# Kernel tuning notes

Hardware: AMD Instinct MI355X
Metric: run time of the kernel (lower is better)

Reference implementation:

```python
import jax, jax.numpy as jnp
import numpy as np

B, L, D = 4, 8192, 256          # batch, seq length, embedding dim
H, HD = 8, 32                   # heads, head dim (H*HD == D)
WN, P, S = 9, 4, 1              # window size, padding, stride
EPS = 1e-5


def _layer_norm(x, g, b):
    m = jnp.mean(x, axis=-1, keepdims=True)
    v = jnp.mean(jnp.square(x - m), axis=-1, keepdims=True)
    return (x - m) / jnp.sqrt(v + EPS) * g + b


def setup_inputs() -> dict:
    key = jax.random.key(0)
    ks = jax.random.split(key, 8)
    sc = 0.05
    return {
        "x": jax.random.normal(ks[0], (B, L, D), jnp.float32),
        "W_q": jax.random.normal(ks[1], (D, D), jnp.float32) * sc,
        "W_k": jax.random.normal(ks[2], (D, D), jnp.float32) * sc,
        "W_v": jax.random.normal(ks[3], (D, D), jnp.float32) * sc,
        "W_o": jax.random.normal(ks[4], (D, D), jnp.float32) * sc,
        "pos": jax.random.normal(ks[5], (WN, D), jnp.float32) * sc,
        "W_out": jax.random.normal(ks[6], (D, D), jnp.float32) * sc,
        "b_out": jnp.zeros((D,), jnp.float32),
        "g1": jnp.ones((D,), jnp.float32),
        "b1": jnp.zeros((D,), jnp.float32),
        "g2": jnp.ones((D,), jnp.float32),
        "b2": jnp.zeros((D,), jnp.float32),
    }


def reference(x, W_q, W_k, W_v, W_o, pos, W_out, b_out, g1, b1, g2, b2):
    # input_dim == embedding_dim -> no input projection
    padded = jnp.pad(x, ((0, 0), (P, P), (0, 0)))
    nw = (L + 2 * P - WN) // S + 1  # == L for S=1, WN=2P+1
    idx = jnp.arange(nw)[:, None] * S + jnp.arange(WN)[None, :]  # [nw, WN]
    win = padded[:, idx] + pos  # [B, nw, WN, D]

    def proj(w):  # [B, nw, WN, H, HD]
        return jnp.einsum('bnwd,de->bnwe', win, w).reshape(B, nw, WN, H, HD)

    q, k, v = proj(W_q), proj(W_k), proj(W_v)
    scale = 1.0 / (HD ** 0.5)
    scores = jnp.einsum('bnqhd,bnkhd->bnhqk', q, k) * scale  # [B,nw,H,WN,WN]
    attn = jax.nn.softmax(scores, axis=-1)
    # context, summed over query positions within each window (use_mean=False)
    ctx = jnp.einsum('bnhqk,bnkhd->bnhd', attn, v).reshape(B, nw, D)
    skip = x[:, ::S]  # [B, nw, D]
    attn_res = _layer_norm(skip + ctx @ W_o, g1, b1)
    out = _layer_norm(attn_res @ W_out.T + b_out + attn_res, g2, b2)
    return jax.nn.relu(out)
```

## Files before the change

kernel.cpp:

```cpp
#include <hip/hip_runtime.h>
#include <hip/hip_bf16.h>
#include <math.h>

constexpr int NB   = 4;
constexpr int LL   = 8192;
constexpr int DD   = 256;
constexpr int NH   = 8;
constexpr int HDIM = 32;
constexpr int WNN  = 9;
constexpr int PPAD = 4;

constexpr int CW  = 32;
constexpr int RSN = CW + 8;
constexpr int SST = 260;

typedef __attribute__((ext_vector_type(8))) short bf16x8;
typedef __attribute__((ext_vector_type(4))) float f32x4;

__device__ inline short f2bf(float f) {
  __hip_bfloat16 h = __float2bfloat16(f);
  short s; __builtin_memcpy(&s, &h, 2); return s;
}
__device__ inline float bf2f(short s) {
  unsigned u = ((unsigned)(unsigned short)s) << 16;
  float f; __builtin_memcpy(&f, &u, 4); return f;
}

__global__ __launch_bounds__(256) void prep_all(
    const float* __restrict__ x, short* __restrict__ XB,
    const float* __restrict__ Wq, const float* __restrict__ Wk, const float* __restrict__ Wv,
    const float* __restrict__ Wo, const float* __restrict__ Wout,
    short* __restrict__ WqT, short* __restrict__ WkT, short* __restrict__ WvT,
    short* __restrict__ WoT, short* __restrict__ WoutB,
    const float* __restrict__ pos,
    short* __restrict__ PQb, short* __restrict__ PKb, short* __restrict__ PVb) {
  __shared__ float ps[256];
  const int t = threadIdx.x;
  const int bx = blockIdx.x;
  if (bx < 4) {
    const float* W = (bx == 0) ? Wq : (bx == 1) ? Wk : (bx == 2) ? Wv : Wo;
    short* T = (bx == 0) ? WqT : (bx == 1) ? WkT : (bx == 2) ? WvT : WoT;
    for (int k = 0; k < 256; k += 4) {
      short4 o;
      o.x = f2bf(W[(size_t)(k + 0) * 256 + t]);
      o.y = f2bf(W[(size_t)(k + 1) * 256 + t]);
      o.z = f2bf(W[(size_t)(k + 2) * 256 + t]);
      o.w = f2bf(W[(size_t)(k + 3) * 256 + t]);
      *(short4*)&T[(size_t)t * 256 + k] = o;
    }
  } else if (bx == 4) {
    for (int i = t; i < 16384; i += 256) {
      float4 v = *(const float4*)(Wout + (size_t)i * 4);
      short4 o; o.x = f2bf(v.x); o.y = f2bf(v.y); o.z = f2bf(v.z); o.w = f2bf(v.w);
      *(short4*)(WoutB + (size_t)i * 4) = o;
    }
  } else if (bx < 32) {
    const int idx = bx - 5;
    const int wrow = idx % WNN, wh = idx / WNN;
    const float* W = (wh == 0) ? Wq : (wh == 1) ? Wk : Wv;
    short* P = (wh == 0) ? PQb : (wh == 1) ? PKb : PVb;
    ps[t] = pos[wrow * 256 + t];
    __syncthreads();
    float a = 0.f;
    for (int d = 0; d < 256; ++d) a += ps[d] * W[(size_t)d * 256 + t];
    P[wrow * 256 + t] = f2bf(a);
  } else {
    size_t i = ((size_t)(bx - 32) * 256 + t) * 4;
    float4 v = *(const float4*)(x + i);
    short4 o; o.x = f2bf(v.x); o.y = f2bf(v.y); o.z = f2bf(v.z); o.w = f2bf(v.w);
    *(short4*)(XB + i) = o;
  }
}

__global__ __launch_bounds__(256) void qkv_mfma(
    const short* __restrict__ XB,
    const short* __restrict__ WT0, const short* __restrict__ WT1, const short* __restrict__ WT2,
    short* __restrict__ O0, short* __restrict__ O1, short* __restrict__ O2) {
  const int t = threadIdx.x, w = t >> 6, lane = t & 63, q = lane >> 4, m = lane & 15;
  const size_t row0 = (size_t)blockIdx.x * 64;
  const short* WT = (blockIdx.y == 0) ? WT0 : (blockIdx.y == 1) ? WT1 : WT2;
  short* O = (blockIdx.y == 0) ? O0 : (blockIdx.y == 1) ? O1 : O2;

  f32x4 acc[4][4];
#pragma unroll
  for (int i = 0; i < 4; ++i)
#pragma unroll
    for (int j = 0; j < 4; ++j) acc[i][j] = (f32x4){0.f, 0.f, 0.f, 0.f};

  const short* abase = XB + (row0 + m) * (size_t)256 + q * 8;
  const short* bbase = WT + (size_t)(w * 64 + m) * 256 + q * 8;
  bf16x8 a[4], b[4];
#pragma unroll
  for (int i = 0; i < 4; ++i) a[i] = *(const bf16x8*)(abase + (size_t)i * 4096);
#pragma unroll
  for (int j = 0; j < 4; ++j) b[j] = *(const bf16x8*)(bbase + (size_t)j * 4096);
#pragma unroll
  for (int kk = 0; kk < 8; ++kk) {
    bf16x8 an[4], bn[4];
    if (kk < 7) {
#pragma unroll
      for (int i = 0; i < 4; ++i) an[i] = *(const bf16x8*)(abase + (size_t)i * 4096 + (kk + 1) * 32);
#pragma unroll
      for (int j = 0; j < 4; ++j) bn[j] = *(const bf16x8*)(bbase + (size_t)j * 4096 + (kk + 1) * 32);
    }
#pragma unroll
    for (int i = 0; i < 4; ++i)
#pragma unroll
      for (int j = 0; j < 4; ++j)
        acc[i][j] = __builtin_amdgcn_mfma_f32_16x16x32_bf16(a[i], b[j], acc[i][j], 0, 0, 0);
    if (kk < 7) {
#pragma unroll
      for (int i = 0; i < 4; ++i) a[i] = an[i];
#pragma unroll
      for (int j = 0; j < 4; ++j) b[j] = bn[j];
    }
  }
#pragma unroll
  for (int i = 0; i < 4; ++i)
#pragma unroll
    for (int j = 0; j < 4; ++j)
#pragma unroll
      for (int r = 0; r < 4; ++r) {
        size_t row = row0 + i * 16 + q * 4 + r;
        int col = w * 64 + j * 16 + m;
        O[row * 256 + col] = f2bf(acc[i][j][r]);
      }
}

__global__ __launch_bounds__(256, 2) void attn_kernel(
    const short* __restrict__ XQb, const short* __restrict__ XKb, const short* __restrict__ XVb,
    const short* __restrict__ PQb, const short* __restrict__ PKb, const short* __restrict__ PVb,
    short* __restrict__ CTXB) {
  __shared__ short sq[RSN * SST];
  __shared__ short sk[RSN * SST];
  __shared__ short sv[RSN * SST];
  __shared__ short pq[WNN * SST];
  __shared__ short pk[WNN * SST];
  __shared__ short pv[WNN * SST];

  const int t = threadIdx.x;
  const int nblk = LL / CW;
  const int b = blockIdx.x / nblk;
  const int n0 = (blockIdx.x % nblk) * CW;
  const size_t base = (size_t)b * LL * DD;

  const int lq   = t & 63;
  const int gcol = ((((lq & 7) << 3) | (lq >> 3))) * 4;
  const int pcol = ((lq >> 3) << 5) | ((lq & 7) << 2);

#pragma unroll
  for (int i = 0; i < RSN / 4; ++i) {
    int r = (t >> 6) + i * 4;
    int j = n0 - PPAD + r;
    short4 vq = {0, 0, 0, 0}, vk = vq, vv = vq;
    if (j >= 0 && j < LL) {
      size_t off = base + (size_t)j * DD + gcol;
      vq = *(const short4*)(XQb + off);
      vk = *(const short4*)(XKb + off);
      vv = *(const short4*)(XVb + off);
    }
    *(short4*)&sq[r * SST + pcol] = vq;
    *(short4*)&sk[r * SST + pcol] = vk;
    *(short4*)&sv[r * SST + pcol] = vv;
  }
#pragma unroll
  for (int i = 0; i < 3; ++i) {
    int r = (t >> 6) + i * 4;
    if (r < WNN) {
      *(short4*)&pq[r * SST + pcol] = *(const short4*)(PQb + r * DD + gcol);
      *(short4*)&pk[r * SST + pcol] = *(const short4*)(PKb + r * DD + gcol);
      *(short4*)&pv[r * SST + pcol] = *(const short4*)(PVb + r * DD + gcol);
    }
  }
  __syncthreads();

  const int n = t >> 3;
  const int h = t & 7;
  const int hoff = h * HDIM;
  const int hph = h * 4;

  float sc[WNN][WNN];
#pragma unroll
  for (int qi = 0; qi < WNN; ++qi)
#pragma unroll
    for (int ki = 0; ki < WNN; ++ki) sc[qi][ki] = 0.f;

#pragma unroll
  for (int c = 0; c < 8; ++c) {
    const int cph = c * 32 + hph;
    float qv[WNN][4], kv[WNN][4];
#pragma unroll
    for (int r = 0; r < WNN; ++r) {
      short4 xa = *(const short4*)&sq[(n + r) * SST + cph];
      short4 pa = *(const short4*)&pq[r * SST + cph];
      qv[r][0] = bf2f(xa.x) + bf2f(pa.x);
      qv[r][1] = bf2f(xa.y) + bf2f(pa.y);
      qv[r][2] = bf2f(xa.z) + bf2f(pa.z);
      qv[r][3] = bf2f(xa.w) + bf2f(pa.w);
      short4 xb = *(const short4*)&sk[(n + r) * SST + cph];
      short4 pb = *(const short4*)&pk[r * SST + cph];
      kv[r][0] = bf2f(xb.x) + bf2f(pb.x);
      kv[r][1] = bf2f(xb.y) + bf2f(pb.y);
      kv[r][2] = bf2f(xb.z) + bf2f(pb.z);
      kv[r][3] = bf2f(xb.w) + bf2f(pb.w);
    }
#pragma unroll
    for (int qi = 0; qi < WNN; ++qi)
#pragma unroll
      for (int ki = 0; ki < WNN; ++ki)
        sc[qi][ki] += qv[qi][0] * kv[ki][0] + qv[qi][1] * kv[ki][1] +
                      qv[qi][2] * kv[ki][2] + qv[qi][3] * kv[ki][3];
  }

  float cs[WNN];
#pragma unroll
  for (int ki = 0; ki < WNN; ++ki) cs[ki] = 0.f;
  const float scale = 0.17677669529663687f;
#pragma unroll
  for (int qi = 0; qi < WNN; ++qi) {
    float mx = sc[qi][0];
#pragma unroll
    for (int ki = 1; ki < WNN; ++ki) mx = fmaxf(mx, sc[qi][ki]);
    float e[WNN], sum = 0.f;
#pragma unroll
    for (int ki = 0; ki < WNN; ++ki) { e[ki] = __expf((sc[qi][ki] - mx) * scale); sum += e[ki]; }
    float inv = 1.f / sum;
#pragma unroll
    for (int ki = 0; ki < WNN; ++ki) cs[ki] += e[ki] * inv;
  }

#pragma unroll
  for (int c = 0; c < 8; ++c) {
    const int cph = c * 32 + hph;
    float o0 = 0.f, o1 = 0.f, o2 = 0.f, o3 = 0.f;
#pragma unroll
    for (int ki = 0; ki < WNN; ++ki) {
      short4 xv4 = *(const short4*)&sv[(n + ki) * SST + cph];
      short4 pv4 = *(const short4*)&pv[ki * SST + cph];
      float wt = cs[ki];
      o0 += wt * (bf2f(xv4.x) + bf2f(pv4.x));
      o1 += wt * (bf2f(xv4.y) + bf2f(pv4.y));
      o2 += wt * (bf2f(xv4.z) + bf2f(pv4.z));
      o3 += wt * (bf2f(xv4.w) + bf2f(pv4.w));
    }
    short4 os; os.x = f2bf(o0); os.y = f2bf(o1); os.z = f2bf(o2); os.w = f2bf(o3);
    *(short4*)(CTXB + base + (size_t)(n0 + n) * DD + hoff + c * 4) = os;
  }
}


__global__ __launch_bounds__(256) void out_mfma(
    const short* __restrict__ CTXB, const float* __restrict__ X,
    const short* __restrict__ WoT, const short* __restrict__ WoutB,
    const float* __restrict__ bo,
    const float* __restrict__ g1, const float* __restrict__ b1,
    const float* __restrict__ g2, const float* __restrict__ b2,
    float* __restrict__ out) {
  __shared__ short ar[64 * 264];
  __shared__ float ws1[64][4], ws2[64][4];
  __shared__ float msh[64], rsh[64];
  __shared__ float g1s[256], b1s[256], g2s[256], b2s[256], bos[256];
  const int t = threadIdx.x, w = t >> 6, lane = t & 63, q = lane >> 4, m = lane & 15;
  const size_t row0 = (size_t)blockIdx.x * 64;
  g1s[t] = g1[t]; b1s[t] = b1[t]; g2s[t] = g2[t]; b2s[t] = b2[t]; bos[t] = bo[t];

  f32x4 acc[4][4];
#pragma unroll
  for (int i = 0; i < 4; ++i)
#pragma unroll
    for (int j = 0; j < 4; ++j) acc[i][j] = (f32x4){0.f, 0.f, 0.f, 0.f};

  const short* abase = CTXB + (row0 + m) * (size_t)256 + q * 8;
  const short* bbase = WoT + (size_t)(w * 64 + m) * 256 + q * 8;
  {
    bf16x8 a[4], b[4];
#pragma unroll
    for (int i = 0; i < 4; ++i) a[i] = *(const bf16x8*)(abase + (size_t)i * 4096);
#pragma unroll
    for (int j = 0; j < 4; ++j) b[j] = *(const bf16x8*)(bbase + (size_t)j * 4096);
#pragma unroll
    for (int kk = 0; kk < 8; ++kk) {
      bf16x8 an[4], bn[4];
      if (kk < 7) {
#pragma unroll
        for (int i = 0; i < 4; ++i) an[i] = *(const bf16x8*)(abase + (size_t)i * 4096 + (kk + 1) * 32);
#pragma unroll
        for (int j = 0; j < 4; ++j) bn[j] = *(const bf16x8*)(bbase + (size_t)j * 4096 + (kk + 1) * 32);
      }
#pragma unroll
      for (int i = 0; i < 4; ++i)
#pragma unroll
        for (int j = 0; j < 4; ++j)
          acc[i][j] = __builtin_amdgcn_mfma_f32_16x16x32_bf16(a[i], b[j], acc[i][j], 0, 0, 0);
      if (kk < 7) {
#pragma unroll
        for (int i = 0; i < 4; ++i) a[i] = an[i];
#pragma unroll
        for (int j = 0; j < 4; ++j) b[j] = bn[j];
      }
    }
  }

  float s1v[4][4], s2v[4][4];
#pragma unroll
  for (int i = 0; i < 4; ++i)
#pragma unroll
    for (int r = 0; r < 4; ++r) {
      float a0 = 0.f, b0 = 0.f;
#pragma unroll
      for (int j = 0; j < 4; ++j) {
        float v = acc[i][j][r] + X[(row0 + i * 16 + q * 4 + r) * 256 + w * 64 + j * 16 + m];
        acc[i][j][r] = v; a0 += v; b0 += v * v;
      }
      s1v[i][r] = a0; s2v[i][r] = b0;
    }
#pragma unroll
  for (int i = 0; i < 4; ++i)
#pragma unroll
    for (int r = 0; r < 4; ++r)
#pragma unroll
      for (int msk = 1; msk < 16; msk <<= 1) {
        s1v[i][r] += __shfl_xor(s1v[i][r], msk, 64);
        s2v[i][r] += __shfl_xor(s2v[i][r], msk, 64);
      }
  if (m == 0) {
#pragma unroll
    for (int i = 0; i < 4; ++i)
#pragma unroll
      for (int r = 0; r < 4; ++r) {
        ws1[i * 16 + q * 4 + r][w] = s1v[i][r];
        ws2[i * 16 + q * 4 + r][w] = s2v[i][r];
      }
  }
  __syncthreads();
  if (t < 64) {
    float a0 = 0.f, b0 = 0.f;
#pragma unroll
    for (int ww = 0; ww < 4; ++ww) { a0 += ws1[t][ww]; b0 += ws2[t][ww]; }
    float mean = a0 * (1.f / 256.f);
    float var = b0 * (1.f / 256.f) - mean * mean;
    msh[t] = mean; rsh[t] = rsqrtf(var + 1e-5f);
  }
  __syncthreads();

#pragma unroll
  for (int i = 0; i < 4; ++i)
#pragma unroll
    for (int r = 0; r < 4; ++r) {
      int row = i * 16 + q * 4 + r;
      float mean = msh[row], rst = rsh[row];
#pragma unroll
      for (int j = 0; j < 4; ++j) {
        int col = w * 64 + j * 16 + m;
        float v = (acc[i][j][r] - mean) * rst * g1s[col] + b1s[col];
        ar[row * 264 + col] = f2bf(v);
      }
    }
  __syncthreads();

#pragma unroll
  for (int i = 0; i < 4; ++i)
#pragma unroll
    for (int j = 0; j < 4; ++j) acc[i][j] = (f32x4){0.f, 0.f, 0.f, 0.f};
  const short* b2base = WoutB + (size_t)(w * 64 + m) * 256 + q * 8;
  {
    bf16x8 b[4];
#pragma unroll
    for (int j = 0; j < 4; ++j) b[j] = *(const bf16x8*)(b2base + (size_t)j * 4096);
#pragma unroll
    for (int kk = 0; kk < 8; ++kk) {
      bf16x8 bn[4];
      if (kk < 7) {
#pragma unroll
        for (int j = 0; j < 4; ++j) bn[j] = *(const bf16x8*)(b2base + (size_t)j * 4096 + (kk + 1) * 32);
      }
      bf16x8 a[4];
#pragma unroll
      for (int i = 0; i < 4; ++i) a[i] = *(const bf16x8*)&ar[(i * 16 + m) * 264 + kk * 32 + q * 8];
#pragma unroll
      for (int i = 0; i < 4; ++i)
#pragma unroll
        for (int j = 0; j < 4; ++j)
          acc[i][j] = __builtin_amdgcn_mfma_f32_16x16x32_bf16(a[i], b[j], acc[i][j], 0, 0, 0);
      if (kk < 7) {
#pragma unroll
        for (int j = 0; j < 4; ++j) b[j] = bn[j];
      }
    }
  }

#pragma unroll
  for (int i = 0; i < 4; ++i)
#pragma unroll
    for (int r = 0; r < 4; ++r) {
      int row = i * 16 + q * 4 + r;
      float a0 = 0.f, b0 = 0.f;
#pragma unroll
      for (int j = 0; j < 4; ++j) {
        int col = w * 64 + j * 16 + m;
        float v = acc[i][j][r] + bos[col] + bf2f(ar[row * 264 + col]);
        acc[i][j][r] = v; a0 += v; b0 += v * v;
      }
      s1v[i][r] = a0; s2v[i][r] = b0;
    }
#pragma unroll
  for (int i = 0; i < 4; ++i)
#pragma unroll
    for (int r = 0; r < 4; ++r)
#pragma unroll
      for (int msk = 1; msk < 16; msk <<= 1) {
        s1v[i][r] += __shfl_xor(s1v[i][r], msk, 64);
        s2v[i][r] += __shfl_xor(s2v[i][r], msk, 64);
      }
  if (m == 0) {
#pragma unroll
    for (int i = 0; i < 4; ++i)
#pragma unroll
      for (int r = 0; r < 4; ++r) {
        ws1[i * 16 + q * 4 + r][w] = s1v[i][r];
        ws2[i * 16 + q * 4 + r][w] = s2v[i][r];
      }
  }
  __syncthreads();
  if (t < 64) {
    float a0 = 0.f, b0 = 0.f;
#pragma unroll
    for (int ww = 0; ww < 4; ++ww) { a0 += ws1[t][ww]; b0 += ws2[t][ww]; }
    float mean = a0 * (1.f / 256.f);
    float var = b0 * (1.f / 256.f) - mean * mean;
    msh[t] = mean; rsh[t] = rsqrtf(var + 1e-5f);
  }
  __syncthreads();

#pragma unroll
  for (int i = 0; i < 4; ++i)
#pragma unroll
    for (int r = 0; r < 4; ++r) {
      int row = i * 16 + q * 4 + r;
      float mean = msh[row], rst = rsh[row];
#pragma unroll
      for (int j = 0; j < 4; ++j) {
        int col = w * 64 + j * 16 + m;
        float v = (acc[i][j][r] - mean) * rst * g2s[col] + b2s[col];
        out[(row0 + row) * 256 + col] = fmaxf(v, 0.f);
      }
    }
}

extern "C" void kernel_launch(void* const* d_in, const int* in_sizes, int n_in,
                              void* d_out, int out_size, void* d_ws, size_t ws_size,
                              hipStream_t stream) {
  const float* x    = (const float*)d_in[0];
  const float* Wq   = (const float*)d_in[1];
  const float* Wk   = (const float*)d_in[2];
  const float* Wv   = (const float*)d_in[3];
  const float* Wo   = (const float*)d_in[4];
  const float* pos  = (const float*)d_in[5];
  const float* Wout = (const float*)d_in[6];
  const float* bo   = (const float*)d_in[7];
  const float* g1   = (const float*)d_in[8];
  const float* b1   = (const float*)d_in[9];
  const float* g2   = (const float*)d_in[10];
  const float* b2   = (const float*)d_in[11];
  float* out = (float*)d_out;

  const size_t nel = (size_t)NB * LL * DD;
  char* wsb = (char*)d_ws;
  short* XB   = (short*)wsb; wsb += nel * 2;
  short* XQb  = (short*)wsb; wsb += nel * 2;
  short* XKb  = (short*)wsb; wsb += nel * 2;
  short* XVb  = (short*)wsb; wsb += nel * 2;
  short* CTXB = (short*)wsb; wsb += nel * 2;
  short* WqT   = (short*)wsb; wsb += 65536 * 2;
  short* WkT   = (short*)wsb; wsb += 65536 * 2;
  short* WvT   = (short*)wsb; wsb += 65536 * 2;
  short* WoT   = (short*)wsb; wsb += 65536 * 2;
  short* WoutB = (short*)wsb; wsb += 65536 * 2;
  short* PQb = (short*)wsb; wsb += WNN * DD * 2;
  short* PKb = (short*)wsb; wsb += WNN * DD * 2;
  short* PVb = (short*)wsb; wsb += WNN * DD * 2;

  prep_all<<<(unsigned)(32 + nel / 4 / 256), 256, 0, stream>>>(
      x, XB, Wq, Wk, Wv, Wo, Wout, WqT, WkT, WvT, WoT, WoutB, pos, PQb, PKb, PVb);
  qkv_mfma<<<dim3((unsigned)(NB * LL / 64), 3), 256, 0, stream>>>(XB, WqT, WkT, WvT, XQb, XKb, XVb);
  attn_kernel<<<NB * (LL / CW), 256, 0, stream>>>(XQb, XKb, XVb, PQb, PKb, PVb, CTXB);
  out_mfma<<<(unsigned)(NB * LL / 64), 256, 0, stream>>>(CTXB, x, WoT, WoutB, bo, g1, b1, g2, b2, out);
}
```

Measured before the change: 257.8 us.

## Split attention query rows across two thread halves with shared-memory reduction

Doubles the attention block to 512 threads. Each (window, head) pair is now handled by two threads, one taking the even query rows and the other the odd ones, and their softmax column sums are combined through a shared buffer that reuses the pq/pk storage. The value-weighting loop is also split by channel halves. This cuts per-thread register pressure (the 9x9 score array drops to 5x9) and raises the number of active threads, at the cost of recomputing the key vectors in both halves and adding extra barriers.

Result: slower. 572.8 us (+122.2%).

```diff
diff --git a/kernel.cpp b/kernel.cpp
--- a/kernel.cpp
+++ b/kernel.cpp
@@ -127,16 +127,17 @@
       }
 }
 
-__global__ __launch_bounds__(256, 2) void attn_kernel(
+__global__ __launch_bounds__(512, 2) void attn_kernel(
     const short* __restrict__ XQb, const short* __restrict__ XKb, const short* __restrict__ XVb,
     const short* __restrict__ PQb, const short* __restrict__ PKb, const short* __restrict__ PVb,
     short* __restrict__ CTXB) {
   __shared__ short sq[RSN * SST];
   __shared__ short sk[RSN * SST];
   __shared__ short sv[RSN * SST];
-  __shared__ short pq[WNN * SST];
-  __shared__ short pk[WNN * SST];
+  __shared__ float csx[2340];
   __shared__ short pv[WNN * SST];
+  short* pq = (short*)csx;
+  short* pk = pq + WNN * SST;
 
   const int t = threadIdx.x;
   const int nblk = LL / CW;
@@ -149,8 +150,8 @@
   const int pcol = ((lq >> 3) << 5) | ((lq & 7) << 2);
 
 #pragma unroll
-  for (int i = 0; i < RSN / 4; ++i) {
-    int r = (t >> 6) + i * 4;
+  for (int i = 0; i < 5; ++i) {
+    int r = (t >> 6) + i * 8;
     int j = n0 - PPAD + r;
     short4 vq = {0, 0, 0, 0}, vk = vq, vv = vq;
     if (j >= 0 && j < LL) {
@@ -164,8 +165,8 @@
     *(short4*)&sv[r * SST + pcol] = vv;
   }
 #pragma unroll
-  for (int i = 0; i < 3; ++i) {
-    int r = (t >> 6) + i * 4;
+  for (int i = 0; i < 2; ++i) {
+    int r = (t >> 6) + i * 8;
     if (r < WNN) {
       *(short4*)&pq[r * SST + pcol] = *(const short4*)(PQb + r * DD + gcol);
       *(short4*)&pk[r * SST + pcol] = *(const short4*)(PKb + r * DD + gcol);
@@ -174,29 +175,26 @@
   }
   __syncthreads();
 
-  const int n = t >> 3;
-  const int h = t & 7;
+  const int p    = t & 255;
+  const int n    = p >> 3;
+  const int h    = p & 7;
+  const int half = t >> 8;
+  const int nq   = 5 - half;
   const int hoff = h * HDIM;
-  const int hph = h * 4;
-
-  float sc[WNN][WNN];
-#pragma unroll
-  for (int qi = 0; qi < WNN; ++qi)
+  const int hph  = h * 4;
+
+  float sc[5][9];
+#pragma unroll
+  for (int qi = 0; qi < 5; ++qi)
 #pragma unroll
     for (int ki = 0; ki < WNN; ++ki) sc[qi][ki] = 0.f;
 
 #pragma unroll
   for (int c = 0; c < 8; ++c) {
     const int cph = c * 32 + hph;
-    float qv[WNN][4], kv[WNN][4];
+    float kv[WNN][4];
 #pragma unroll
     for (int r = 0; r < WNN; ++r) {
-      short4 xa = *(const short4*)&sq[(n + r) * SST + cph];
-      short4 pa = *(const short4*)&pq[r * SST + cph];
-      qv[r][0] = bf2f(xa.x) + bf2f(pa.x);
-      qv[r][1] = bf2f(xa.y) + bf2f(pa.y);
-      qv[r][2] = bf2f(xa.z) + bf2f(pa.z);
-      qv[r][3] = bf2f(xa.w) + bf2f(pa.w);
       short4 xb = *(const short4*)&sk[(n + r) * SST + cph];
       short4 pb = *(const short4*)&pk[r * SST + cph];
       kv[r][0] = bf2f(xb.x) + bf2f(pb.x);
@@ -204,12 +202,28 @@
       kv[r][2] = bf2f(xb.z) + bf2f(pb.z);
       kv[r][3] = bf2f(xb.w) + bf2f(pb.w);
     }
-#pragma unroll
-    for (int qi = 0; qi < WNN; ++qi)
-#pragma unroll
-      for (int ki = 0; ki < WNN; ++ki)
-        sc[qi][ki] += qv[qi][0] * kv[ki][0] + qv[qi][1] * kv[ki][1] +
-                      qv[qi][2] * kv[ki][2] + qv[qi][3] * kv[ki][3];
+    float qv[5][4];
+#pragma unroll
+    for (int idx = 0; idx < 5; ++idx) {
+      if (idx < nq) {
+        int r = 2 * idx + half;
+        short4 xa = *(const short4*)&sq[(n + r) * SST + cph];
+        short4 pa = *(const short4*)&pq[r * SST + cph];
+        qv[idx][0] = bf2f(xa.x) + bf2f(pa.x);
+        qv[idx][1] = bf2f(xa.y) + bf2f(pa.y);
+        qv[idx][2] = bf2f(xa.z) + bf2f(pa.z);
+        qv[idx][3] = bf2f(xa.w) + bf2f(pa.w);
+      }
+    }
+#pragma unroll
+    for (int idx = 0; idx < 5; ++idx) {
+      if (idx < nq) {
+#pragma unroll
+        for (int ki = 0; ki < WNN; ++ki)
+          sc[idx][ki] += qv[idx][0] * kv[ki][0] + qv[idx][1] * kv[ki][1] +
+                         qv[idx][2] * kv[ki][2] + qv[idx][3] * kv[ki][3];
+      }
+    }
   }
 
   float cs[WNN];
@@ -217,21 +231,42 @@
   for (int ki = 0; ki < WNN; ++ki) cs[ki] = 0.f;
   const float scale = 0.17677669529663687f;
 #pragma unroll
-  for (int qi = 0; qi < WNN; ++qi) {
-    float mx = sc[qi][0];
-#pragma unroll
-    for (int ki = 1; ki < WNN; ++ki) mx = fmaxf(mx, sc[qi][ki]);
-    float e[WNN], sum = 0.f;
-#pragma unroll
-    for (int ki = 0; ki < WNN; ++ki) { e[ki] = __expf((sc[qi][ki] - mx) * scale); sum += e[ki]; }
-    float inv = 1.f / sum;
-#pragma unroll
-    for (int ki = 0; ki < WNN; ++ki) cs[ki] += e[ki] * inv;
-  }
-
-#pragma unroll
-  for (int c = 0; c < 8; ++c) {
-    const int cph = c * 32 + hph;
+  for (int idx = 0; idx < 5; ++idx) {
+    if (idx < nq) {
+      float mx = sc[idx][0];
+#pragma unroll
+      for (int ki = 1; ki < WNN; ++ki) mx = fmaxf(mx, sc[idx][ki]);
+      float e[WNN], sum = 0.f;
+#pragma unroll
+      for (int ki = 0; ki < WNN; ++ki) { e[ki] = __expf((sc[idx][ki] - mx) * scale); sum += e[ki]; }
+      float inv = 1.f / sum;
+#pragma unroll
+      for (int ki = 0; ki < WNN; ++ki) cs[ki] += e[ki] * inv;
+    }
+  }
+
+  __syncthreads();
+  if (half == 1) {
+#pragma unroll
+    for (int ki = 0; ki < WNN; ++ki) csx[p * WNN + ki] = cs[ki];
+  }
+  __syncthreads();
+  if (half == 0) {
+#pragma unroll
+    for (int ki = 0; ki < WNN; ++ki) cs[ki] += csx[p * WNN + ki];
+#pragma unroll
+    for (int ki = 0; ki < WNN; ++ki) csx[p * WNN + ki] = cs[ki];
+  }
+  __syncthreads();
+  if (half == 1) {
+#pragma unroll
+    for (int ki = 0; ki < WNN; ++ki) cs[ki] = csx[p * WNN + ki];
+  }
+
+#pragma unroll
+  for (int c = 0; c < 4; ++c) {
+    const int cc = half * 4 + c;
+    const int cph = cc * 32 + hph;
     float o0 = 0.f, o1 = 0.f, o2 = 0.f, o3 = 0.f;
 #pragma unroll
     for (int ki = 0; ki < WNN; ++ki) {
@@ -244,7 +279,7 @@
       o3 += wt * (bf2f(xv4.w) + bf2f(pv4.w));
     }
     short4 os; os.x = f2bf(o0); os.y = f2bf(o1); os.z = f2bf(o2); os.w = f2bf(o3);
-    *(short4*)(CTXB + base + (size_t)(n0 + n) * DD + hoff + c * 4) = os;
+    *(short4*)(CTXB + base + (size_t)(n0 + n) * DD + hoff + cc * 4) = os;
   }
 }
 
@@ -483,6 +518,6 @@
   prep_all<<<(unsigned)(32 + nel / 4 / 256), 256, 0, stream>>>(
       x, XB, Wq, Wk, Wv, Wo, Wout, WqT, WkT, WvT, WoT, WoutB, pos, PQb, PKb, PVb);
   qkv_mfma<<<dim3((unsigned)(NB * LL / 64), 3), 256, 0, stream>>>(XB, WqT, WkT, WvT, XQb, XKb, XVb);
-  attn_kernel<<<NB * (LL / CW), 256, 0, stream>>>(XQb, XKb, XVb, PQb, PKb, PVb, CTXB);
+  attn_kernel<<<NB * (LL / CW), 512, 0, stream>>>(XQb, XKb, XVb, PQb, PKb, PVb, CTXB);
   out_mfma<<<(unsigned)(NB * LL / 64), 256, 0, stream>>>(CTXB, x, WoT, WoutB, bo, g1, b1, g2, b2, out);
 }
```
